# Performance work log

Measured on AMD Instinct MI355X. Metric: run time of the kernel, lower is better.

Reference implementation:

```python
import jax, jax.numpy as jnp
import numpy as np

NUM_HEADS = 16
HEAD_SIZE = 64
N_EMBD = 1024
BLOCK_SIZE = 2048
B, T = 4, 2048


def setup_inputs() -> dict:
    key = jax.random.key(0)
    ks = jax.random.split(key, 6)
    scale = (N_EMBD * NUM_HEADS) ** (-0.5)
    x = jax.random.normal(ks[0], (B, T, N_EMBD), dtype=jnp.float32)
    Wk = jax.random.normal(ks[1], (NUM_HEADS, N_EMBD, HEAD_SIZE), dtype=jnp.float32) * scale
    Wq = jax.random.normal(ks[2], (NUM_HEADS, N_EMBD, HEAD_SIZE), dtype=jnp.float32) * scale
    Wv = jax.random.normal(ks[3], (NUM_HEADS, N_EMBD, HEAD_SIZE), dtype=jnp.float32) * scale
    proj_w = jax.random.normal(ks[4], (N_EMBD, N_EMBD), dtype=jnp.float32) * (N_EMBD ** -0.5)
    proj_b = jax.random.normal(ks[5], (N_EMBD,), dtype=jnp.float32) * 0.01
    return {"x": x, "Wk": Wk, "Wq": Wq, "Wv": Wv, "proj_w": proj_w, "proj_b": proj_b}


def reference(x, Wk, Wq, Wv, proj_w, proj_b):
    Bsz, Tlen, C = x.shape
    # per-head projections: x [b,t,c] @ W [h,c,d] -> [b,h,t,d]
    q = jnp.einsum('btc,hcd->bhtd', x, Wq)
    k = jnp.einsum('btc,hcd->bhtd', x, Wk)
    v = jnp.einsum('btc,hcd->bhtd', x, Wv)
    wei = jnp.einsum('bhtd,bhsd->bhts', q, k) * (HEAD_SIZE ** -0.5)
    causal = jnp.tril(jnp.ones((Tlen, Tlen), dtype=bool))  # [T,T]
    wei = jnp.where(causal[None, None, :, :], wei, -jnp.inf)
    wei = jax.nn.softmax(wei, axis=-1)
    out = jnp.einsum('bhts,bhsd->bhtd', wei, v)
    out = out.transpose(0, 2, 1, 3).reshape(Bsz, Tlen, NUM_HEADS * HEAD_SIZE)
    out = out @ proj_w.T + proj_b  # nn.Linear: x W^T + b
    return out
```

## Files before the change

### kernel.cpp

```cpp
#include <hip/hip_runtime.h>
#include <hip/hip_bf16.h>

#define BB 4
#define TT 2048
#define CC 1024
#define HH 16
#define DD 64
#define MM (BB * TT)
#define NN_QKV 3072

typedef __attribute__((ext_vector_type(8))) short short8;
typedef __attribute__((ext_vector_type(4))) short short4v;
typedef __attribute__((ext_vector_type(4))) int i32x4;
typedef __attribute__((ext_vector_type(4))) float f32x4;
typedef __attribute__((ext_vector_type(16))) float f32x16;

static __device__ __forceinline__ float exp2_hw(float x) {
  return __builtin_amdgcn_exp2f(x);
}

static __device__ __forceinline__ short f2bf(float f) {
  __hip_bfloat16 h = __float2bfloat16(f);
  short s;
  __builtin_memcpy(&s, &h, 2);
  return s;
}

static __device__ __forceinline__ unsigned int pack2(float a, float b) {
  unsigned int lo = (unsigned short)f2bf(a);
  unsigned int hi = (unsigned short)f2bf(b);
  return lo | (hi << 16);
}

static __device__ __forceinline__ f32x16 zero16() {
  f32x16 z;
#pragma unroll
  for (int i = 0; i < 16; ++i) z[i] = 0.f;
  return z;
}

static __device__ __forceinline__ int swzv(int d) {
  return (((d & 7) ^ ((d >> 3) & 7)) << 4);
}

static __device__ __forceinline__ void gld16(const void* g, void* l) {
  __builtin_amdgcn_global_load_lds(
      (const __attribute__((address_space(1))) unsigned int*)g,
      (__attribute__((address_space(3))) unsigned int*)l, 16, 0, 0);
}

__global__ __launch_bounds__(256) void cvt8_kernel(const float* __restrict__ in,
                                                   short* __restrict__ out, int n8) {
  int i = blockIdx.x * 256 + threadIdx.x;
  if (i >= n8) return;
  const float4 a = ((const float4*)in)[i * 2];
  const float4 b = ((const float4*)in)[i * 2 + 1];
  short8 o;
  o[0] = f2bf(a.x); o[1] = f2bf(a.y); o[2] = f2bf(a.z); o[3] = f2bf(a.w);
  o[4] = f2bf(b.x); o[5] = f2bf(b.y); o[6] = f2bf(b.z); o[7] = f2bf(b.w);
  ((short8*)out)[i] = o;
}

__global__ __launch_bounds__(256) void cvtw_kernel(
    const float* __restrict__ Wq, const float* __restrict__ Wk,
    const float* __restrict__ Wv, short* __restrict__ Wt) {
  __shared__ float tile[64][65];
  const int tid = threadIdx.x;
  const int h = blockIdx.x;
  const int c0 = blockIdx.y * 64;
  const int sel = blockIdx.z;
  const float* W = (sel == 0) ? Wq : (sel == 1) ? Wk : Wv;

#pragma unroll
  for (int it = 0; it < 16; ++it) {
    int e = it * 256 + tid;
    int cc = e >> 6, d = e & 63;
    tile[d][cc] = W[((size_t)h * CC + c0 + cc) * DD + d];
  }
  __syncthreads();
#pragma unroll
  for (int it = 0; it < 16; ++it) {
    int e = it * 256 + tid;
    int d = e >> 6, cc = e & 63;
    Wt[((size_t)((sel * 16 + h) * 64 + d)) * CC + c0 + cc] = f2bf(tile[d][cc]);
  }
}

template <int MODE>
__global__ __launch_bounds__(256) void mfma_gemm_kernel(
    const short* __restrict__ A, const short* __restrict__ Bt,
    const float* __restrict__ bias,
    __hip_bfloat16* __restrict__ Oq, __hip_bfloat16* __restrict__ Ok,
    __hip_bfloat16* __restrict__ Ov, float* __restrict__ Of) {
  __shared__ __align__(16) short Als[128 * 32];
  __shared__ __align__(16) short Bls[128 * 32];

  const int tid = threadIdx.x;
  const int w = tid >> 6, l = tid & 63;
  const int lg = l >> 4, ll = l & 15;
  const int wr = w >> 1, wc = w & 1;
  const int m0 = blockIdx.x * 128;
  const int n0 = blockIdx.y * 128;

  const int row0 = tid >> 2, kc0 = (tid & 3) * 8;
  const int row1 = (tid + 256) >> 2, kc1 = (tid & 3) * 8;

  f32x4 acc[4][4] = {};

  for (int kt = 0; kt < CC; kt += 32) {
    __syncthreads();
    gld16(A + (size_t)(m0 + row0) * CC + kt + kc0, (char*)Als + w * 1024);
    gld16(A + (size_t)(m0 + row1) * CC + kt + kc1, (char*)Als + 4096 + w * 1024);
    gld16(Bt + (size_t)(n0 + row0) * CC + kt + kc0, (char*)Bls + w * 1024);
    gld16(Bt + (size_t)(n0 + row1) * CC + kt + kc1, (char*)Bls + 4096 + w * 1024);
    __syncthreads();

    short8 af[4], bfr[4];
#pragma unroll
    for (int i = 0; i < 4; ++i)
      af[i] = *(const short8*)&Als[(wr * 64 + i * 16 + ll) * 32 + lg * 8];
#pragma unroll
    for (int j = 0; j < 4; ++j)
      bfr[j] = *(const short8*)&Bls[(wc * 64 + j * 16 + ll) * 32 + lg * 8];
#pragma unroll
    for (int i = 0; i < 4; ++i)
#pragma unroll
      for (int j = 0; j < 4; ++j)
        acc[i][j] = __builtin_amdgcn_mfma_f32_16x16x32_bf16(af[i], bfr[j], acc[i][j], 0, 0, 0);
  }

  if (MODE == 0) {
    const int b = m0 >> 11;
#pragma unroll
    for (int j = 0; j < 4; ++j) {
      const int nbase = n0 + wc * 64 + j * 16;
      const int sel = nbase >> 10;
      const int h = (nbase >> 6) & 15;
      const int d = (nbase & 63) + ll;
      __hip_bfloat16* O = (sel == 0) ? Oq : (sel == 1) ? Ok : Ov;
      const float sc = (sel == 0) ? 0.18033688011112042f : 1.0f;
#pragma unroll
      for (int i = 0; i < 4; ++i) {
#pragma unroll
        for (int r = 0; r < 4; ++r) {
          const int t = (m0 + wr * 64 + i * 16 + lg * 4 + r) & (TT - 1);
          O[(((size_t)b * HH + h) * TT + t) * DD + d] = __float2bfloat16(acc[i][j][r] * sc);
        }
      }
    }
  } else {
#pragma unroll
    for (int j = 0; j < 4; ++j) {
      const int n = n0 + wc * 64 + j * 16 + ll;
      const float bv = bias[n];
#pragma unroll
      for (int i = 0; i < 4; ++i) {
#pragma unroll
        for (int r = 0; r < 4; ++r) {
          const int m = m0 + wr * 64 + i * 16 + lg * 4 + r;
          Of[(size_t)m * CC + n] = acc[i][j][r] + bv;
        }
      }
    }
  }
}

__global__ __launch_bounds__(512) void attn32_kernel(
    const __hip_bfloat16* __restrict__ qg, const __hip_bfloat16* __restrict__ kg,
    const __hip_bfloat16* __restrict__ vg, __hip_bfloat16* __restrict__ att) {
  __shared__ __align__(16) char LDS[34816];
  char* Ks = LDS;
  char* Vt0 = LDS + 16384;
  char* Vt1 = LDS + 24576;

  const int tid = threadIdx.x;
  const int w = tid >> 6, l = tid & 63;
  const int l31 = l & 31, hi = l >> 5;
  const int w4 = w & 3, g = w >> 2;

  const int flat = blockIdx.x;
  const int r_ = flat >> 6;
  const int qt = (r_ < 4) ? (15 - r_) : (r_ < 8) ? (r_ + 4)
               : (r_ < 12) ? (15 - r_) : (r_ - 12);
  const int hb = flat & 63;
  const int h = hb & 15, b = hb >> 4;
  const size_t base = ((size_t)b * HH + h) * TT * DD;

  const int q0w = qt * 128 + w4 * 32;
  const int myq = q0w + l31;

  const short* Kg = (const short*)kg + base;
  const short* Vg = (const short*)vg + base;
  const int kr = tid >> 3;
  const int kc = tid & 7;
  const int vs = tid >> 3;
  const int vd0 = (tid & 7) * 8;

  const short* Qp = (const short*)qg + base + (size_t)myq * DD;
  const short8 qf0 = *(const short8*)(Qp + 0 + hi * 8);
  const short8 qf1 = *(const short8*)(Qp + 16 + hi * 8);
  const short8 qf2 = *(const short8*)(Qp + 32 + hi * 8);
  const short8 qf3 = *(const short8*)(Qp + 48 + hi * 8);

  f32x16 o0 = zero16(), o1 = zero16();
  float lsum = 0.f;

  const int npair = qt + 1;

#pragma unroll 1
  for (int pt = 0; pt < npair; ++pt) {
    const int sb = pt * 128;

    gld16(Kg + (size_t)(sb + kr) * DD + ((kc ^ (kr & 7)) * 8), Ks + w * 1024);
    gld16(Kg + (size_t)(sb + kr + 64) * DD + ((kc ^ (kr & 7)) * 8),
          Ks + 8192 + w * 1024);
    const short8 va = *(const short8*)(Vg + (size_t)(sb + vs) * DD + vd0);
    const short8 vb = *(const short8*)(Vg + (size_t)(sb + 64 + vs) * DD + vd0);
#pragma unroll
    for (int e = 0; e < 8; ++e) {
      const int d = vd0 + e;
      *(short*)(Vt0 + d * 128 + ((vs * 2) ^ swzv(d))) = va[e];
      *(short*)(Vt1 + d * 128 + ((vs * 2) ^ swzv(d))) = vb[e];
    }
    __syncthreads();

    const int sbg = sb + g * 64;
    const char* Vtg = g ? Vt1 : Vt0;
#pragma unroll
    for (int ks = 0; ks < 2; ++ks) {
      const int sbh = sbg + ks * 32;
      if (sbh > q0w + 31) continue;

      const int krow = g * 64 + ks * 32 + l31;
      const char* Kr = Ks + krow * 128;
      const int rsz = (krow & 7) << 4;
      const short8 kf0 = *(const short8*)(Kr + ((0 * 32 + hi * 16) ^ rsz));
      const short8 kf1 = *(const short8*)(Kr + ((1 * 32 + hi * 16) ^ rsz));
      const short8 kf2 = *(const short8*)(Kr + ((2 * 32 + hi * 16) ^ rsz));
      const short8 kf3 = *(const short8*)(Kr + ((3 * 32 + hi * 16) ^ rsz));
      f32x16 sT = zero16();
      __builtin_amdgcn_s_setprio(1);
      sT = __builtin_amdgcn_mfma_f32_32x32x16_bf16(kf0, qf0, sT, 0, 0, 0);
      sT = __builtin_amdgcn_mfma_f32_32x32x16_bf16(kf1, qf1, sT, 0, 0, 0);
      sT = __builtin_amdgcn_mfma_f32_32x32x16_bf16(kf2, qf2, sT, 0, 0, 0);
      sT = __builtin_amdgcn_mfma_f32_32x32x16_bf16(kf3, qf3, sT, 0, 0, 0);
      __builtin_amdgcn_s_setprio(0);

      float p[16];
      if (sbh == q0w) {
#pragma unroll
        for (int r = 0; r < 16; ++r) {
          const int sg = sbh + (r & 3) + 8 * (r >> 2) + 4 * hi;
          p[r] = (sg > myq) ? -INFINITY : sT[r];
        }
      } else {
#pragma unroll
        for (int r = 0; r < 16; ++r) p[r] = sT[r];
      }

      float ps = 0.f;
#pragma unroll
      for (int r = 0; r < 16; ++r) {
        p[r] = exp2_hw(p[r]);
        ps += p[r];
      }
      lsum += ps;

      unsigned int W[4][2], X[4][2];
#pragma unroll
      for (int qd = 0; qd < 4; ++qd) {
        W[qd][0] = pack2(p[4 * qd + 0], p[4 * qd + 1]);
        W[qd][1] = pack2(p[4 * qd + 2], p[4 * qd + 3]);
        X[qd][0] = __shfl_xor((int)W[qd][0], 32);
        X[qd][1] = __shfl_xor((int)W[qd][1], 32);
      }

#pragma unroll
      for (int kst = 0; kst < 2; ++kst) {
        union { i32x4 i; short8 s; } A;
        A.i[0] = hi ? (int)X[2 * kst + 1][0] : (int)W[2 * kst][0];
        A.i[1] = hi ? (int)X[2 * kst + 1][1] : (int)W[2 * kst][1];
        A.i[2] = hi ? (int)W[2 * kst + 1][0] : (int)X[2 * kst][0];
        A.i[3] = hi ? (int)W[2 * kst + 1][1] : (int)X[2 * kst][1];
        const int kb = (ks * 32 + kst * 16 + hi * 8) * 2;
        const int r0 = l31, r1 = 32 + l31;
        const short8 vf0 = *(const short8*)(Vtg + r0 * 128 + (kb ^ swzv(r0)));
        const short8 vf1 = *(const short8*)(Vtg + r1 * 128 + (kb ^ swzv(r1)));
        __builtin_amdgcn_s_setprio(1);
        o0 = __builtin_amdgcn_mfma_f32_32x32x16_bf16(vf0, A.s, o0, 0, 0, 0);
        o1 = __builtin_amdgcn_mfma_f32_32x32x16_bf16(vf1, A.s, o1, 0, 0, 0);
        __builtin_amdgcn_s_setprio(0);
      }
    }
    __syncthreads();
  }

  lsum += __shfl_xor(lsum, 32);

  float* comb = (float*)LDS;
  const int idx17 = (w4 * 64 + l) * 17;
  if (g == 1) {
#pragma unroll
    for (int i = 0; i < 16; ++i) comb[idx17 + i] = o0[i];
    comb[idx17 + 16] = lsum;
  }
  __syncthreads();
  if (g == 0) {
#pragma unroll
    for (int i = 0; i < 16; ++i) o0[i] += comb[idx17 + i];
    lsum += comb[idx17 + 16];
  }
  __syncthreads();
  const int idx16 = (w4 * 64 + l) * 16;
  if (g == 1) {
#pragma unroll
    for (int i = 0; i < 16; ++i) comb[idx16 + i] = o1[i];
  }
  __syncthreads();
  if (g == 0) {
#pragma unroll
    for (int i = 0; i < 16; ++i) o1[i] += comb[idx16 + i];

    const float inv = 1.0f / lsum;
    short* orow = (short*)att + ((size_t)b * TT + myq) * CC + h * DD;
#pragma unroll
    for (int j = 0; j < 4; ++j) {
      short4v s0, s1;
#pragma unroll
      for (int i = 0; i < 4; ++i) {
        s0[i] = f2bf(o0[4 * j + i] * inv);
        s1[i] = f2bf(o1[4 * j + i] * inv);
      }
      *(short4v*)(orow + 8 * j + 4 * hi) = s0;
      *(short4v*)(orow + 32 + 8 * j + 4 * hi) = s1;
    }
  }
}

extern "C" void kernel_launch(void* const* d_in, const int* in_sizes, int n_in,
                              void* d_out, int out_size, void* d_ws, size_t ws_size,
                              hipStream_t stream) {
  const float* x  = (const float*)d_in[0];
  const float* Wk = (const float*)d_in[1];
  const float* Wq = (const float*)d_in[2];
  const float* Wv = (const float*)d_in[3];
  const float* pw = (const float*)d_in[4];
  const float* pb = (const float*)d_in[5];
  float* out = (float*)d_out;

  const size_t QE = (size_t)BB * HH * TT * DD;
  __hip_bfloat16* q   = (__hip_bfloat16*)d_ws;
  __hip_bfloat16* k   = q + QE;
  __hip_bfloat16* v   = k + QE;
  short* xbf          = (short*)(v + QE);
  __hip_bfloat16* att = (__hip_bfloat16*)xbf;
  short* Wt           = xbf + QE;
  short* pwbf         = Wt;

  cvt8_kernel<<<(MM * CC / 8 + 255) / 256, 256, 0, stream>>>(x, xbf, MM * CC / 8);
  cvtw_kernel<<<dim3(HH, CC / 64, 3), 256, 0, stream>>>(Wq, Wk, Wv, Wt);
  mfma_gemm_kernel<0><<<dim3(MM / 128, NN_QKV / 128), 256, 0, stream>>>(
      xbf, Wt, nullptr, q, k, v, nullptr);
  attn32_kernel<<<dim3(1024, 1, 1), 512, 0, stream>>>(q, k, v, att);
  cvt8_kernel<<<(CC * CC / 8 + 255) / 256, 256, 0, stream>>>(pw, pwbf, CC * CC / 8);
  mfma_gemm_kernel<1><<<dim3(MM / 128, CC / 128), 256, 0, stream>>>(
      (const short*)att, pwbf, pb, nullptr, nullptr, nullptr, out);
}
```

Before: 163.5 us.

## Replace QKV GEMM with 256x256 double-buffered swizzled-LDS MFMA kernel

Adds a dedicated QKV projection kernel that computes 256x256 tiles with 8 waves and a K-step of 64. It double-buffers A/B tiles in 128KB of LDS, issuing the next tile's global loads while the current tile's MFMAs run. An XOR swizzle on the LDS layout avoids bank conflicts, and s_setprio raises wave priority around the MFMA bursts. The 128KB LDS footprint and the register pressure from 32 accumulators per thread limit occupancy, and the grid shrinks to 32x12 blocks. The output projection keeps the old kernel, split out as a non-templated copy.

```diff
diff --git a/kernel.cpp b/kernel.cpp
--- a/kernel.cpp
+++ b/kernel.cpp
@@ -86,12 +86,127 @@
   }
 }
 
-template <int MODE>
-__global__ __launch_bounds__(256) void mfma_gemm_kernel(
+__global__ __launch_bounds__(512, 2) void qkv256_kernel(
     const short* __restrict__ A, const short* __restrict__ Bt,
-    const float* __restrict__ bias,
     __hip_bfloat16* __restrict__ Oq, __hip_bfloat16* __restrict__ Ok,
-    __hip_bfloat16* __restrict__ Ov, float* __restrict__ Of) {
+    __hip_bfloat16* __restrict__ Ov) {
+  __shared__ __align__(16) char LDS[131072];
+
+  const int tid = threadIdx.x;
+  const int w = tid >> 6, l = tid & 63;
+  const int ll = l & 15, lg = l >> 4;
+  const int wm = w >> 2, wn = w & 3;
+  const int m0 = blockIdx.x * 256;
+  const int n0 = blockIdx.y * 256;
+
+  const int srow = tid >> 3;
+  const int schunk = tid & 7;
+  const int sswz = (schunk ^ (srow & 7)) * 8;
+
+  f32x4 acc[8][4];
+#pragma unroll
+  for (int i = 0; i < 8; ++i)
+#pragma unroll
+    for (int j = 0; j < 4; ++j) acc[i][j] = f32x4{0.f, 0.f, 0.f, 0.f};
+
+#pragma unroll
+  for (int i = 0; i < 4; ++i) {
+    gld16(A + (size_t)(m0 + i * 64 + srow) * CC + sswz, LDS + i * 8192 + w * 1024);
+    gld16(Bt + (size_t)(n0 + i * 64 + srow) * CC + sswz,
+          LDS + 32768 + i * 8192 + w * 1024);
+  }
+  __syncthreads();
+
+  int cur = 0;
+#pragma unroll 1
+  for (int kt = 0; kt < CC; kt += 64) {
+    const char* Ab = LDS + cur * 65536;
+    const char* Bb = Ab + 32768;
+    const char* nbase_lds = LDS + (cur ^ 1) * 65536;
+    const bool haveNext = (kt + 64 < CC);
+    const int ktn = kt + 64;
+
+    short8 bfrag[4][2];
+#pragma unroll
+    for (int p = 0; p < 4; ++p) {
+      if (p == 0) {
+#pragma unroll
+        for (int n = 0; n < 4; ++n) {
+          const int rowB = wn * 64 + n * 16 + ll;
+#pragma unroll
+          for (int k = 0; k < 2; ++k)
+            bfrag[n][k] = *(const short8*)(Bb + rowB * 128 +
+                                           (((k * 4 + lg) ^ (ll & 7)) * 16));
+        }
+      }
+      short8 afrag[2][2];
+#pragma unroll
+      for (int i = 0; i < 2; ++i) {
+        const int rowA = wm * 128 + (2 * p + i) * 16 + ll;
+#pragma unroll
+        for (int k = 0; k < 2; ++k)
+          afrag[i][k] = *(const short8*)(Ab + rowA * 128 +
+                                         (((k * 4 + lg) ^ (ll & 7)) * 16));
+      }
+
+      if (haveNext) {
+        if (p < 2) {
+          const int i0 = p * 2, i1 = p * 2 + 1;
+          gld16(A + (size_t)(m0 + i0 * 64 + srow) * CC + ktn + sswz,
+                (char*)nbase_lds + i0 * 8192 + w * 1024);
+          gld16(A + (size_t)(m0 + i1 * 64 + srow) * CC + ktn + sswz,
+                (char*)nbase_lds + i1 * 8192 + w * 1024);
+        } else {
+          const int i0 = (p - 2) * 2, i1 = (p - 2) * 2 + 1;
+          gld16(Bt + (size_t)(n0 + i0 * 64 + srow) * CC + ktn + sswz,
+                (char*)nbase_lds + 32768 + i0 * 8192 + w * 1024);
+          gld16(Bt + (size_t)(n0 + i1 * 64 + srow) * CC + ktn + sswz,
+                (char*)nbase_lds + 32768 + i1 * 8192 + w * 1024);
+        }
+      }
+
+      __builtin_amdgcn_s_barrier();
+      __builtin_amdgcn_s_setprio(1);
+#pragma unroll
+      for (int i = 0; i < 2; ++i)
+#pragma unroll
+        for (int n = 0; n < 4; ++n)
+#pragma unroll
+          for (int k = 0; k < 2; ++k)
+            acc[2 * p + i][n] = __builtin_amdgcn_mfma_f32_16x16x32_bf16(
+                afrag[i][k], bfrag[n][k], acc[2 * p + i][n], 0, 0, 0);
+      __builtin_amdgcn_s_setprio(0);
+      if (p < 3) __builtin_amdgcn_s_barrier();
+    }
+
+    __syncthreads();
+    cur ^= 1;
+  }
+
+  const int b = m0 >> 11;
+#pragma unroll
+  for (int n = 0; n < 4; ++n) {
+    const int nbase = n0 + wn * 64 + n * 16;
+    const int sel = nbase >> 10;
+    const int h = (nbase >> 6) & 15;
+    const int d = (nbase & 63) + ll;
+    __hip_bfloat16* O = (sel == 0) ? Oq : (sel == 1) ? Ok : Ov;
+    const float sc = (sel == 0) ? 0.18033688011112042f : 1.0f;
+#pragma unroll
+    for (int i = 0; i < 8; ++i) {
+#pragma unroll
+      for (int r = 0; r < 4; ++r) {
+        const int t = (m0 + wm * 128 + i * 16 + lg * 4 + r) & (TT - 1);
+        O[(((size_t)b * HH + h) * TT + t) * DD + d] =
+            __float2bfloat16(acc[i][n][r] * sc);
+      }
+    }
+  }
+}
+
+__global__ __launch_bounds__(256) void proj_gemm_kernel(
+    const short* __restrict__ A, const short* __restrict__ Bt,
+    const float* __restrict__ bias, float* __restrict__ Of) {
   __shared__ __align__(16) short Als[128 * 32];
   __shared__ __align__(16) short Bls[128 * 32];
 
@@ -129,37 +244,16 @@
         acc[i][j] = __builtin_amdgcn_mfma_f32_16x16x32_bf16(af[i], bfr[j], acc[i][j], 0, 0, 0);
   }
 
-  if (MODE == 0) {
-    const int b = m0 >> 11;
-#pragma unroll
-    for (int j = 0; j < 4; ++j) {
-      const int nbase = n0 + wc * 64 + j * 16;
-      const int sel = nbase >> 10;
-      const int h = (nbase >> 6) & 15;
-      const int d = (nbase & 63) + ll;
-      __hip_bfloat16* O = (sel == 0) ? Oq : (sel == 1) ? Ok : Ov;
-      const float sc = (sel == 0) ? 0.18033688011112042f : 1.0f;
-#pragma unroll
-      for (int i = 0; i < 4; ++i) {
-#pragma unroll
-        for (int r = 0; r < 4; ++r) {
-          const int t = (m0 + wr * 64 + i * 16 + lg * 4 + r) & (TT - 1);
-          O[(((size_t)b * HH + h) * TT + t) * DD + d] = __float2bfloat16(acc[i][j][r] * sc);
-        }
-      }
-    }
-  } else {
-#pragma unroll
-    for (int j = 0; j < 4; ++j) {
-      const int n = n0 + wc * 64 + j * 16 + ll;
-      const float bv = bias[n];
-#pragma unroll
-      for (int i = 0; i < 4; ++i) {
-#pragma unroll
-        for (int r = 0; r < 4; ++r) {
-          const int m = m0 + wr * 64 + i * 16 + lg * 4 + r;
-          Of[(size_t)m * CC + n] = acc[i][j][r] + bv;
-        }
+#pragma unroll
+  for (int j = 0; j < 4; ++j) {
+    const int n = n0 + wc * 64 + j * 16 + ll;
+    const float bv = bias[n];
+#pragma unroll
+    for (int i = 0; i < 4; ++i) {
+#pragma unroll
+      for (int r = 0; r < 4; ++r) {
+        const int m = m0 + wr * 64 + i * 16 + lg * 4 + r;
+        Of[(size_t)m * CC + n] = acc[i][j][r] + bv;
       }
     }
   }
@@ -359,10 +453,10 @@
 
   cvt8_kernel<<<(MM * CC / 8 + 255) / 256, 256, 0, stream>>>(x, xbf, MM * CC / 8);
   cvtw_kernel<<<dim3(HH, CC / 64, 3), 256, 0, stream>>>(Wq, Wk, Wv, Wt);
-  mfma_gemm_kernel<0><<<dim3(MM / 128, NN_QKV / 128), 256, 0, stream>>>(
-      xbf, Wt, nullptr, q, k, v, nullptr);
+  qkv256_kernel<<<dim3(MM / 256, NN_QKV / 256), 512, 0, stream>>>(
+      xbf, Wt, q, k, v);
   attn32_kernel<<<dim3(1024, 1, 1), 512, 0, stream>>>(q, k, v, att);
   cvt8_kernel<<<(CC * CC / 8 + 255) / 256, 256, 0, stream>>>(pw, pwbf, CC * CC / 8);
-  mfma_gemm_kernel<1><<<dim3(MM / 128, CC / 128), 256, 0, stream>>>(
-      (const short*)att, pwbf, pb, nullptr, nullptr, nullptr, out);
-}
+  proj_gemm_kernel<<<dim3(MM / 128, CC / 128), 256, 0, stream>>>(
+      (const short*)att, pwbf, pb, out);
+}
```

New measurement: 166.0 us. About the same (+1.5%).
